# Kernel optimization log

Measured on AMD Instinct MI355X. Metric: run time of the kernel, lower is better.

## Reference

```python
import jax, jax.numpy as jnp
import numpy as np

N_NODES = 100000
F_IN = 128
F_HID = 64  # gcn_filters = [64, 64]
MLP_HID = 128


def setup_inputs() -> dict:
    key = jax.random.key(0)
    ks = jax.random.split(key, 12)
    E, Q = 3200000, 1000000
    feature = jax.random.normal(ks[0], (N_NODES, F_IN), dtype=jnp.float32)
    edges = jax.random.randint(ks[1], (2, E), 0, N_NODES, dtype=jnp.int32)
    i = jax.random.randint(ks[2], (Q,), 0, N_NODES, dtype=jnp.int32)
    j = jax.random.randint(ks[3], (Q,), 0, N_NODES, dtype=jnp.int32)
    s = lambda d: 1.0 / jnp.sqrt(d)
    W1 = jax.random.normal(ks[4], (F_IN, F_HID), dtype=jnp.float32) * s(F_IN)
    b1 = jnp.zeros((F_HID,), dtype=jnp.float32)
    W2 = jax.random.normal(ks[5], (F_HID, F_HID), dtype=jnp.float32) * s(F_HID)
    b2 = jnp.zeros((F_HID,), dtype=jnp.float32)
    fc1_W = jax.random.normal(ks[6], (2 * F_HID, MLP_HID), dtype=jnp.float32) * s(2 * F_HID)
    fc1_b = jnp.zeros((MLP_HID,), dtype=jnp.float32)
    fc2_W = jax.random.normal(ks[7], (MLP_HID, 2), dtype=jnp.float32) * s(MLP_HID)
    fc2_b = jnp.zeros((2,), dtype=jnp.float32)
    return {"feature": feature, "edges": edges, "i": i, "j": j,
            "W1": W1, "b1": b1, "W2": W2, "b2": b2,
            "fc1_W": fc1_W, "fc1_b": fc1_b, "fc2_W": fc2_W, "fc2_b": fc2_b}


def _gcn_layer(x, W, b, src, dst, norm, n):
    h = x @ W
    msg = h[src] * norm[:, None]
    return jax.ops.segment_sum(msg, dst, num_segments=n) + b


def reference(feature, edges, i, j, W1, b1, W2, b2, fc1_W, fc1_b, fc2_W, fc2_b):
    n = feature.shape[0]
    loops = jnp.arange(n, dtype=edges.dtype)
    src = jnp.concatenate([edges[0], loops])
    dst = jnp.concatenate([edges[1], loops])
    deg = jax.ops.segment_sum(jnp.ones(src.shape[0], feature.dtype), dst, num_segments=n)
    dinv = jax.lax.rsqrt(jnp.maximum(deg, 1e-12))
    norm = dinv[src] * dinv[dst]
    h = jax.nn.relu(_gcn_layer(feature, W1, b1, src, dst, norm, n))
    out = _gcn_layer(h, W2, b2, src, dst, norm, n)  # [N, F_HID]
    embd = jnp.concatenate([out[i], out[j]], axis=-1)  # [Q, 2*F_HID]
    hid = jax.nn.relu(embd @ fc1_W + fc1_b)
    return hid @ fc2_W + fc2_b
```

## Files before the change

kernel.cpp:

```cpp
#include <hip/hip_runtime.h>
#include <hip/hip_bf16.h>
#include <hip/hip_fp16.h>
#include <cstdint>

#define F_IN 128
#define F_HID 64
#define NB 64
#define MAXB 2048
#define NWG 1024
#define PREPB 16

typedef _Float16 half8 __attribute__((ext_vector_type(8)));
typedef float floatx4 __attribute__((ext_vector_type(4)));

__device__ __forceinline__ float bf2f(unsigned short u) {
  return __uint_as_float(((unsigned int)u) << 16);
}
__device__ __forceinline__ unsigned short f2bf(float f) {
  unsigned int u = __float_as_uint(f);
  u += 0x7FFFu + ((u >> 16) & 1u);
  return (unsigned short)(u >> 16);
}
__device__ __forceinline__ float h2f(unsigned short u) {
  return __half2float(__ushort_as_half(u));
}
__device__ __forceinline__ unsigned short f2h(float f) {
  return __half_as_ushort(__float2half(f));
}

__global__ __launch_bounds__(64) void k_detect(const unsigned int* __restrict__ Xw,
                                               int* __restrict__ flag) {
  int lane = threadIdx.x;
  int cnt = 0;
  for (int t = lane; t < 256; t += 64) {
    unsigned int ex = (Xw[t] >> 7) & 0xFFu;
    cnt += (ex >= 117u && ex <= 137u) ? 1 : 0;
  }
#pragma unroll
  for (int off = 32; off > 0; off >>= 1) cnt += __shfl_xor(cnt, off, 64);
  if (lane == 0) *flag = (cnt >= 128) ? 1 : 0;
}

__global__ __launch_bounds__(256) void k_front(const void* __restrict__ Xv,
                                               unsigned short* __restrict__ Xh, int total8,
                                               const void* __restrict__ W1v,
                                               const void* __restrict__ W2v,
                                               const void* __restrict__ fc1Wv,
                                               unsigned short* __restrict__ fW1,
                                               unsigned short* __restrict__ fW2,
                                               unsigned short* __restrict__ fPR,
                                               const int* __restrict__ dst,
                                               int* __restrict__ hist, int E, int B, int chunk,
                                               const int* __restrict__ flagp) {
  __shared__ int lh[MAXB];
  const int bid = blockIdx.x;
  if (bid < NWG) {
    int w = bid, tid = threadIdx.x;
    for (int b = tid; b < B; b += 256) lh[b] = 0;
    __syncthreads();
    int e0 = w * chunk, e1 = min(E, e0 + chunk);
    for (int e = e0 + tid; e < e1; e += 256) atomicAdd(&lh[dst[e] >> 6], 1);
    __syncthreads();
    for (int b = tid; b < B; b += 256) hist[w * B + b] = lh[b];
    return;
  }
  const bool isb = (*flagp != 0);
  if (bid < NWG + PREPB) {
    int tid = (bid - NWG) * 256 + threadIdx.x;
    int stride = PREPB * 256;
    for (int e = tid; e < F_IN * F_HID; e += stride) {
      int k = e >> 6, n = e & 63;
      unsigned short v = isb ? f2h(bf2f(((const unsigned short*)W1v)[e]))
                             : f2h(((const float*)W1v)[e]);
      int c = k >> 5, q = (k >> 3) & 3, j = k & 7, t = n >> 4, m = n & 15;
      fW1[((c * 4 + t) * 64 + q * 16 + m) * 8 + j] = v;
    }
    for (int e = tid; e < F_HID * F_HID; e += stride) {
      int k = e >> 6, n = e & 63;
      unsigned short v = isb ? f2h(bf2f(((const unsigned short*)W2v)[e]))
                             : f2h(((const float*)W2v)[e]);
      int c = k >> 5, q = (k >> 3) & 3, j = k & 7, t = n >> 4, m = n & 15;
      fW2[((c * 4 + t) * 64 + q * 16 + m) * 8 + j] = v;
    }
    for (int ge = tid; ge < 4 * F_HID * 64; ge += stride) {
      int g = ge >> 12, e = ge & 4095;
      int k = e >> 6, n = e & 63;
      int src = (((g & 2) ? 64 : 0) + k) * 128 + (g & 1) * 64 + n;
      unsigned short v = isb ? f2h(bf2f(((const unsigned short*)fc1Wv)[src]))
                             : f2h(((const float*)fc1Wv)[src]);
      int c = k >> 5, q = (k >> 3) & 3, j = k & 7, t = n >> 4, m = n & 15;
      fPR[g * 4096 + ((c * 4 + t) * 64 + q * 16 + m) * 8 + j] = v;
    }
    return;
  }
  int t = (bid - (NWG + PREPB)) * 256 + threadIdx.x;
  int stride = (gridDim.x - (NWG + PREPB)) * 256;
  for (; t < total8; t += stride) {
    unsigned short r[8];
    if (isb) {
      uint4 d = reinterpret_cast<const uint4*>(Xv)[t];
      r[0] = f2h(__uint_as_float(d.x << 16));
      r[1] = f2h(__uint_as_float(d.x & 0xFFFF0000u));
      r[2] = f2h(__uint_as_float(d.y << 16));
      r[3] = f2h(__uint_as_float(d.y & 0xFFFF0000u));
      r[4] = f2h(__uint_as_float(d.z << 16));
      r[5] = f2h(__uint_as_float(d.z & 0xFFFF0000u));
      r[6] = f2h(__uint_as_float(d.w << 16));
      r[7] = f2h(__uint_as_float(d.w & 0xFFFF0000u));
    } else {
      float4 a = reinterpret_cast<const float4*>(Xv)[2 * t];
      float4 b = reinterpret_cast<const float4*>(Xv)[2 * t + 1];
      r[0] = f2h(a.x); r[1] = f2h(a.y); r[2] = f2h(a.z); r[3] = f2h(a.w);
      r[4] = f2h(b.x); r[5] = f2h(b.y); r[6] = f2h(b.z); r[7] = f2h(b.w);
    }
    uint4 o;
    o.x = (unsigned int)r[0] | ((unsigned int)r[1] << 16);
    o.y = (unsigned int)r[2] | ((unsigned int)r[3] << 16);
    o.z = (unsigned int)r[4] | ((unsigned int)r[5] << 16);
    o.w = (unsigned int)r[6] | ((unsigned int)r[7] << 16);
    reinterpret_cast<uint4*>(Xh)[t] = o;
  }
}

__global__ __launch_bounds__(256) void k_bscan1(int* __restrict__ hist,
                                                int* __restrict__ btot, int B) {
  int b = (blockIdx.x * 256 + threadIdx.x) >> 6;
  int lane = threadIdx.x & 63;
  if (b >= B) return;
  int v[16];
  int s = 0;
#pragma unroll
  for (int k = 0; k < 16; k++) {
    v[k] = hist[(size_t)(lane * 16 + k) * B + b];
    s += v[k];
  }
  int pre = s;
#pragma unroll
  for (int off = 1; off < 64; off <<= 1) {
    int t = __shfl_up(pre, off, 64);
    if (lane >= off) pre += t;
  }
  int running = pre - s;
#pragma unroll
  for (int k = 0; k < 16; k++) {
    int val = v[k];
    hist[(size_t)(lane * 16 + k) * B + b] = running;
    running += val;
  }
  if (lane == 63) btot[b] = running;
}

__global__ __launch_bounds__(256) void k_bscan2(const int* __restrict__ btot,
                                                int* __restrict__ boff, int B, int E) {
  __shared__ int partial[256];
  int t = threadIdx.x;
  int CH = (B + 255) / 256;
  int b0 = t * CH, b1 = min(B, b0 + CH);
  int tt = 0;
  for (int b = b0; b < b1; b++) tt += btot[b];
  partial[t] = tt;
  __syncthreads();
  if (t == 0) {
    int acc = 0;
    for (int i = 0; i < 256; i++) { int v = partial[i]; partial[i] = acc; acc += v; }
  }
  __syncthreads();
  int off = partial[t];
  for (int b = b0; b < b1; b++) { boff[b] = off; off += btot[b]; }
  if (t == 255) boff[B] = E;
}

__global__ __launch_bounds__(256) void k_bfill(const int* __restrict__ src,
                                               const int* __restrict__ dst,
                                               const int* __restrict__ hist,
                                               const int* __restrict__ boff,
                                               int* __restrict__ buck,
                                               int E, int B, int chunk) {
  __shared__ int cur[MAXB];
  int w = blockIdx.x, tid = threadIdx.x;
  for (int b = tid; b < B; b += 256) cur[b] = boff[b] + hist[w * B + b];
  __syncthreads();
  int e0 = w * chunk, e1 = min(E, e0 + chunk);
  for (int e = e0 + tid; e < e1; e += 256) {
    int d = dst[e];
    int b = d >> 6, dl = d & 63;
    int p = atomicAdd(&cur[b], 1);
    buck[p] = (dl << 17) | src[e];
  }
}

__global__ __launch_bounds__(256) void k_bsort(const int* __restrict__ buck,
                                               const int* __restrict__ boff,
                                               int* __restrict__ csr,
                                               int* __restrict__ noff,
                                               float* __restrict__ dinv, int N) {
  __shared__ int bin[NB][4];
  __shared__ int excl[NB];
  int b = blockIdx.x, tid = threadIdx.x;
  const int rep = tid & 3;
  for (int i = tid; i < NB * 4; i += 256) ((int*)bin)[i] = 0;
  __syncthreads();
  int r0 = boff[b], r1 = boff[b + 1];
  for (int r = r0 + tid; r < r1; r += 256) atomicAdd(&bin[buck[r] >> 17][rep], 1);
  __syncthreads();
  if (tid < NB)
    excl[tid] = bin[tid][0] + bin[tid][1] + bin[tid][2] + bin[tid][3];
  __syncthreads();
  if (tid == 0) {
    int acc = 0;
    for (int i = 0; i < NB; i++) { int v = excl[i]; excl[i] = acc; acc += v; }
  }
  __syncthreads();
  if (tid < NB) {
    int n = b * NB + tid;
    int c0 = bin[tid][0], c1 = bin[tid][1], c2 = bin[tid][2], c3 = bin[tid][3];
    if (n < N) {
      dinv[n] = rsqrtf((float)(c0 + c1 + c2 + c3) + 1.0f);
      noff[n] = r0 + excl[tid];
    }
    int base = excl[tid];
    bin[tid][0] = base;
    bin[tid][1] = base + c0;
    bin[tid][2] = base + c0 + c1;
    bin[tid][3] = base + c0 + c1 + c2;
  }
  if (b == gridDim.x - 1 && tid == 128) noff[N] = r1;
  __syncthreads();
  for (int r = r0 + tid; r < r1; r += 256) {
    int rec = buck[r];
    int p = atomicAdd(&bin[rec >> 17][rep], 1);
    csr[r0 + p] = rec & 0x1FFFF;
  }
}


__global__ __launch_bounds__(256, 4) void k_gemm1(const unsigned short* __restrict__ Xh,
                                                  const unsigned short* __restrict__ fW1,
                                                  const float* __restrict__ dinv,
                                                  unsigned short* __restrict__ G, int N) {
  int tid = threadIdx.x;
  const int lane = tid & 63, wave = tid >> 6;
  const int m = lane & 15, q = lane >> 4;
  half8 bfrag[4][4];
#pragma unroll
  for (int c = 0; c < 4; c++)
#pragma unroll
    for (int t = 0; t < 4; t++)
      bfrag[c][t] = *reinterpret_cast<const half8*>(fW1 + ((c * 4 + t) * 64 + lane) * 8);
  int ntiles = (N + 15) >> 4;
  for (int tile = blockIdx.x * 4 + wave; tile < ntiles; tile += gridDim.x * 4) {
    int r0 = tile << 4;
    int rm = r0 + m; rm = rm < N ? rm : N - 1;
    floatx4 acc[4] = {{0.f,0.f,0.f,0.f},{0.f,0.f,0.f,0.f},{0.f,0.f,0.f,0.f},{0.f,0.f,0.f,0.f}};
#pragma unroll
    for (int c = 0; c < 4; c++) {
      half8 a = *reinterpret_cast<const half8*>(Xh + (size_t)rm * F_IN + c * 32 + q * 8);
#pragma unroll
      for (int t = 0; t < 4; t++)
        acc[t] = __builtin_amdgcn_mfma_f32_16x16x32_f16(a, bfrag[c][t], acc[t], 0, 0, 0);
    }
#pragma unroll
    for (int rr = 0; rr < 4; rr++) {
      int grow = r0 + q * 4 + rr;
      if (grow < N) {
        float dv = dinv[grow];
#pragma unroll
        for (int t = 0; t < 4; t++)
          G[(size_t)grow * F_HID + t * 16 + m] = f2h(acc[t][rr] * dv);
      }
    }
  }
}

__global__ __launch_bounds__(256, 4) void k_gemm2(const unsigned short* __restrict__ O,
                                                  const unsigned short* __restrict__ fW2,
                                                  const float* __restrict__ dinv,
                                                  unsigned short* __restrict__ G, int N) {
  int tid = threadIdx.x;
  const int lane = tid & 63, wave = tid >> 6;
  const int m = lane & 15, q = lane >> 4;
  half8 bfrag[2][4];
#pragma unroll
  for (int c = 0; c < 2; c++)
#pragma unroll
    for (int t = 0; t < 4; t++)
      bfrag[c][t] = *reinterpret_cast<const half8*>(fW2 + ((c * 4 + t) * 64 + lane) * 8);
  int ntiles = (N + 15) >> 4;
  for (int tile = blockIdx.x * 4 + wave; tile < ntiles; tile += gridDim.x * 4) {
    int r0 = tile << 4;
    int rm = r0 + m; rm = rm < N ? rm : N - 1;
    floatx4 acc[4] = {{0.f,0.f,0.f,0.f},{0.f,0.f,0.f,0.f},{0.f,0.f,0.f,0.f},{0.f,0.f,0.f,0.f}};
#pragma unroll
    for (int c = 0; c < 2; c++) {
      half8 a = *reinterpret_cast<const half8*>(O + (size_t)rm * F_HID + c * 32 + q * 8);
#pragma unroll
      for (int t = 0; t < 4; t++)
        acc[t] = __builtin_amdgcn_mfma_f32_16x16x32_f16(a, bfrag[c][t], acc[t], 0, 0, 0);
    }
#pragma unroll
    for (int rr = 0; rr < 4; rr++) {
      int grow = r0 + q * 4 + rr;
      if (grow < N) {
        float dv = dinv[grow];
#pragma unroll
        for (int t = 0; t < 4; t++)
          G[(size_t)grow * F_HID + t * 16 + m] = f2h(acc[t][rr] * dv);
      }
    }
  }
}

template <bool RELU>
__global__ __launch_bounds__(256) void k_agg(const int* __restrict__ csr,
                                             const int* __restrict__ noff,
                                             const unsigned short* __restrict__ H,
                                             const float* __restrict__ dinv,
                                             const void* __restrict__ bias,
                                             unsigned short* __restrict__ OUT, int N,
                                             const int* __restrict__ flagp) {
  const bool isb = (*flagp != 0);
  const int lane = threadIdx.x & 63;
  const int g = lane >> 4, l16 = lane & 15;
  const int gw = (blockIdx.x * 256 + threadIdx.x) >> 6;
  const int nW = (gridDim.x * 256) >> 6;
  float bv[4];
#pragma unroll
  for (int d = 0; d < 4; d++)
    bv[d] = isb ? bf2f(((const unsigned short*)bias)[l16 * 4 + d])
                : ((const float*)bias)[l16 * 4 + d];
  for (int n = gw; n < N; n += nW) {
    int start = noff[n], end = noff[n + 1];
    float a0 = 0.f, a1 = 0.f, a2 = 0.f, a3 = 0.f;
    for (int e0 = start; e0 < end; e0 += 64) {
      int ee = e0 + lane;
      int idx = (ee < end) ? csr[ee] : 0;
      int m = end - e0; m = m < 64 ? m : 64;
      int nc = m >> 2;
      int c = 0;
      for (; c + 8 <= nc; c += 8) {
        int s[8];
#pragma unroll
        for (int u = 0; u < 8; u++) s[u] = __shfl(idx, (c + u) * 4 + g, 64);
        ushort4 v[8];
#pragma unroll
        for (int u = 0; u < 8; u++)
          v[u] = *reinterpret_cast<const ushort4*>(H + (size_t)s[u] * F_HID + l16 * 4);
#pragma unroll
        for (int u = 0; u < 8; u++) {
          a0 += h2f(v[u].x); a1 += h2f(v[u].y);
          a2 += h2f(v[u].z); a3 += h2f(v[u].w);
        }
      }
      for (; c < nc; c++) {
        int s0 = __shfl(idx, c * 4 + g, 64);
        ushort4 v0 = *reinterpret_cast<const ushort4*>(H + (size_t)s0 * F_HID + l16 * 4);
        a0 += h2f(v0.x); a1 += h2f(v0.y); a2 += h2f(v0.z); a3 += h2f(v0.w);
      }
      int rem = m & 3;
      if (rem) {
        int s0 = __shfl(idx, nc * 4 + g, 64);
        if (g < rem) {
          ushort4 v0 = *reinterpret_cast<const ushort4*>(H + (size_t)s0 * F_HID + l16 * 4);
          a0 += h2f(v0.x); a1 += h2f(v0.y); a2 += h2f(v0.z); a3 += h2f(v0.w);
        }
      }
    }
    a0 += __shfl_xor(a0, 16, 64); a0 += __shfl_xor(a0, 32, 64);
    a1 += __shfl_xor(a1, 16, 64); a1 += __shfl_xor(a1, 32, 64);
    a2 += __shfl_xor(a2, 16, 64); a2 += __shfl_xor(a2, 32, 64);
    a3 += __shfl_xor(a3, 16, 64); a3 += __shfl_xor(a3, 32, 64);
    ushort4 sv = *reinterpret_cast<const ushort4*>(H + (size_t)n * F_HID + l16 * 4);
    float dv = dinv[n];
    float o0 = (a0 + h2f(sv.x)) * dv + bv[0];
    float o1 = (a1 + h2f(sv.y)) * dv + bv[1];
    float o2 = (a2 + h2f(sv.z)) * dv + bv[2];
    float o3 = (a3 + h2f(sv.w)) * dv + bv[3];
    if (RELU) {
      o0 = fmaxf(o0, 0.f); o1 = fmaxf(o1, 0.f);
      o2 = fmaxf(o2, 0.f); o3 = fmaxf(o3, 0.f);
    }
    if (lane < 16) {
      ushort4 ov;
      ov.x = f2h(o0); ov.y = f2h(o1); ov.z = f2h(o2); ov.w = f2h(o3);
      *reinterpret_cast<ushort4*>(OUT + (size_t)n * F_HID + l16 * 4) = ov;
    }
  }
}

__global__ __launch_bounds__(512) void k_query(const unsigned short* __restrict__ O,
                                               const unsigned short* __restrict__ fPR,
                                               const int* __restrict__ qi,
                                               const int* __restrict__ qj,
                                               const void* __restrict__ fc1b,
                                               const void* __restrict__ fc2W,
                                               const void* __restrict__ fc2b,
                                               void* __restrict__ out, int Q,
                                               const int* __restrict__ flagp) {
  __shared__ unsigned short sB[4 * 4096];
  const bool isb = (*flagp != 0);
  int tid = threadIdx.x;
  {
    const uint4* srcp = reinterpret_cast<const uint4*>(fPR);
    uint4* dstp = reinterpret_cast<uint4*>(sB);
#pragma unroll
    for (int r = 0; r < 4; r++) dstp[tid + r * 512] = srcp[tid + r * 512];
  }
  const int lane = tid & 63, wave = tid >> 6;
  const int m_ = lane & 15, qk = lane >> 4;
  float bb[8], w0[8], w1[8];
#pragma unroll
  for (int T = 0; T < 8; T++) {
    int h = T * 16 + m_;
    if (isb) {
      bb[T] = bf2f(((const unsigned short*)fc1b)[h]);
      w0[T] = bf2f(((const unsigned short*)fc2W)[h * 2 + 0]);
      w1[T] = bf2f(((const unsigned short*)fc2W)[h * 2 + 1]);
    } else {
      bb[T] = ((const float*)fc1b)[h];
      w0[T] = ((const float*)fc2W)[h * 2 + 0];
      w1[T] = ((const float*)fc2W)[h * 2 + 1];
    }
  }
  float ob0 = isb ? bf2f(((const unsigned short*)fc2b)[0]) : ((const float*)fc2b)[0];
  float ob1 = isb ? bf2f(((const unsigned short*)fc2b)[1]) : ((const float*)fc2b)[1];
  __syncthreads();
  const half8* sBv = reinterpret_cast<const half8*>(sB);

  const int ntiles = (Q + 15) >> 4;
  const int nW = gridDim.x * 8;
  int tile = blockIdx.x * 8 + wave;
  if (tile >= ntiles) return;

  auto ldidx = [&](int t, int& iq, int& jq) {
    if (t < ntiles) {
      int q = t * 16 + m_;
      int qq = q < Q ? q : Q - 1;
      iq = qi[qq];
      jq = qj[qq];
    }
  };
  auto gather = [&](int iq, int jq, half8& I0, half8& I1, half8& J0, half8& J1) {
    const half8* pI = reinterpret_cast<const half8*>(O + (size_t)iq * F_HID) + qk;
    const half8* pJ = reinterpret_cast<const half8*>(O + (size_t)jq * F_HID) + qk;
    I0 = pI[0]; I1 = pI[4];
    J0 = pJ[0]; J1 = pJ[4];
  };

  int iqn = 0, jqn = 0;
  ldidx(tile, iqn, jqn);
  half8 I0, I1, J0, J1;
  gather(iqn, jqn, I0, I1, J0, J1);
  ldidx(tile + nW, iqn, jqn);

  for (; tile < ntiles; tile += nW) {
    half8 nI0, nI1, nJ0, nJ1;
    gather(iqn, jqn, nI0, nI1, nJ0, nJ1);
    ldidx(tile + 2 * nW, iqn, jqn);

    float r0[4] = {0.f, 0.f, 0.f, 0.f};
    float r1[4] = {0.f, 0.f, 0.f, 0.f};
    const floatx4 zz = {0.f, 0.f, 0.f, 0.f};
#pragma unroll
    for (int h = 0; h < 2; h++) {
      floatx4 acc[4];
#pragma unroll
      for (int tt = 0; tt < 4; tt++) acc[tt] = zz;
      __builtin_amdgcn_s_setprio(1);
#pragma unroll
      for (int tt = 0; tt < 4; tt++) {
        acc[tt] = __builtin_amdgcn_mfma_f32_16x16x32_f16(
            I0, sBv[h * 512 + tt * 64 + lane], acc[tt], 0, 0, 0);
        acc[tt] = __builtin_amdgcn_mfma_f32_16x16x32_f16(
            I1, sBv[h * 512 + (4 + tt) * 64 + lane], acc[tt], 0, 0, 0);
        acc[tt] = __builtin_amdgcn_mfma_f32_16x16x32_f16(
            J0, sBv[(2 + h) * 512 + tt * 64 + lane], acc[tt], 0, 0, 0);
        acc[tt] = __builtin_amdgcn_mfma_f32_16x16x32_f16(
            J1, sBv[(2 + h) * 512 + (4 + tt) * 64 + lane], acc[tt], 0, 0, 0);
      }
      __builtin_amdgcn_s_setprio(0);
#pragma unroll
      for (int tt = 0; tt < 4; tt++) {
        int T = h * 4 + tt;
#pragma unroll
        for (int rr = 0; rr < 4; rr++) {
          float hv = fmaxf(acc[tt][rr] + bb[T], 0.f);
          r0[rr] += hv * w0[T];
          r1[rr] += hv * w1[T];
        }
      }
      __builtin_amdgcn_sched_barrier(0);
    }
#pragma unroll
    for (int rr = 0; rr < 4; rr++) {
      float a0 = r0[rr], a1 = r1[rr];
#pragma unroll
      for (int off = 8; off > 0; off >>= 1) {
        a0 += __shfl_xor(a0, off, 16);
        a1 += __shfl_xor(a1, off, 16);
      }
      if (m_ == 0) {
        int q = tile * 16 + qk * 4 + rr;
        if (q < Q) {
          if (isb) {
            *reinterpret_cast<ushort2*>((unsigned short*)out + (size_t)q * 2) =
                make_ushort2(f2bf(a0 + ob0), f2bf(a1 + ob1));
          } else {
            *reinterpret_cast<float2*>((float*)out + (size_t)q * 2) =
                make_float2(a0 + ob0, a1 + ob1);
          }
        }
      }
    }
    I0 = nI0; I1 = nI1; J0 = nJ0; J1 = nJ1;
  }
}

extern "C" void kernel_launch(void* const* d_in, const int* in_sizes, int n_in,
                              void* d_out, int out_size, void* d_ws, size_t ws_size,
                              hipStream_t stream) {
  const void* X    = d_in[0];
  const int*  edges= (const int*)d_in[1];
  const int*  qi   = (const int*)d_in[2];
  const int*  qj   = (const int*)d_in[3];
  const void* W1   = d_in[4];
  const void* b1   = d_in[5];
  const void* W2   = d_in[6];
  const void* b2   = d_in[7];
  const void* fc1W = d_in[8];
  const void* fc1b = d_in[9];
  const void* fc2W = d_in[10];
  const void* fc2b = d_in[11];

  const int N = in_sizes[0] / F_IN;
  const int E = in_sizes[1] / 2;
  const int Q = in_sizes[2];
  const int B = (N + NB - 1) / NB;
  const int chunk = (E + NWG - 1) / NWG;

  char* ws = (char*)d_ws;
  size_t off = 0;
  auto alloc = [&](size_t bytes) -> void* {
    void* p = ws + off;
    off += (bytes + 255) & ~(size_t)255;
    return p;
  };
  int*            flag = (int*)alloc(4);
  float*          dinv = (float*)alloc((size_t)N * 4);
  unsigned short* Xh   = (unsigned short*)alloc((size_t)N * F_IN * 2);
  unsigned short* G    = (unsigned short*)alloc((size_t)N * F_HID * 2);
  unsigned short* O    = (unsigned short*)alloc((size_t)N * F_HID * 2);
  unsigned short* fW1  = (unsigned short*)alloc((size_t)F_IN * F_HID * 2);
  unsigned short* fW2  = (unsigned short*)alloc((size_t)F_HID * F_HID * 2);
  unsigned short* fPR  = (unsigned short*)alloc((size_t)4 * F_HID * 64 * 2);
  int* hist = (int*)alloc((size_t)NWG * B * 4);
  int* btot = (int*)alloc((size_t)(B + 1) * 4);
  int* boff = (int*)alloc((size_t)(B + 1) * 4);
  int* buck = (int*)alloc((size_t)E * 4);
  int* csr  = (int*)alloc((size_t)E * 4);
  int* noff = (int*)alloc((size_t)(N + 1) * 4);
  (void)ws_size; (void)n_in; (void)out_size;

  const int* esrc = edges;
  const int* edst = edges + E;

  k_detect<<<1, 64, 0, stream>>>((const unsigned int*)X, flag);
  k_front<<<2048, 256, 0, stream>>>(X, Xh, N * F_IN / 8, W1, W2, fc1W, fW1, fW2, fPR,
                                    edst, hist, E, B, chunk, flag);

  k_bscan1<<<(B + 3) / 4, 256, 0, stream>>>(hist, btot, B);
  k_bscan2<<<1, 256, 0, stream>>>(btot, boff, B, E);
  k_bfill<<<NWG, 256, 0, stream>>>(esrc, edst, hist, boff, buck, E, B, chunk);
  k_bsort<<<B, 256, 0, stream>>>(buck, boff, csr, noff, dinv, N);

  k_gemm1<<<2048, 256, 0, stream>>>(Xh, fW1, dinv, G, N);
  k_agg<true><<<2048, 256, 0, stream>>>(csr, noff, G, dinv, b1, O, N, flag);

  k_gemm2<<<2048, 256, 0, stream>>>(O, fW2, dinv, G, N);
  k_agg<false><<<2048, 256, 0, stream>>>(csr, noff, G, dinv, b2, O, N, flag);

  k_query<<<1024, 512, 0, stream>>>(O, fPR, qi, qj, fc1b, fc2W, fc2b, d_out, Q, flag);
}
```

Measured before the change: 450.8 us.

## Stage bucket fill through LDS for coalesced bucketed writes, fewer workgroups

The bucket-fill kernel now sorts each chunk of edges by bucket in shared memory (local histogram, local scan, local scatter) before writing them to global memory. Edges for the same bucket then land in contiguous runs, replacing the random global scatter. The workgroup count drops from 1024 to 256 so each group handles a larger chunk, and the scan kernel is generalized to match. The cost is extra LDS traffic, several barriers per stage, a serial 256-entry scan on one thread, and lower occupancy from the large shared-memory footprint.

```diff
diff --git a/kernel.cpp b/kernel.cpp
--- a/kernel.cpp
+++ b/kernel.cpp
@@ -7,8 +7,9 @@
 #define F_HID 64
 #define NB 64
 #define MAXB 2048
-#define NWG 1024
+#define NWG 256
 #define PREPB 16
+#define STAGE 12800
 
 typedef _Float16 half8 __attribute__((ext_vector_type(8)));
 typedef float floatx4 __attribute__((ext_vector_type(4)));
@@ -124,14 +125,15 @@
 
 __global__ __launch_bounds__(256) void k_bscan1(int* __restrict__ hist,
                                                 int* __restrict__ btot, int B) {
+  const int WPL = NWG / 64;
   int b = (blockIdx.x * 256 + threadIdx.x) >> 6;
   int lane = threadIdx.x & 63;
   if (b >= B) return;
-  int v[16];
+  int v[WPL];
   int s = 0;
 #pragma unroll
-  for (int k = 0; k < 16; k++) {
-    v[k] = hist[(size_t)(lane * 16 + k) * B + b];
+  for (int k = 0; k < WPL; k++) {
+    v[k] = hist[(size_t)(lane * WPL + k) * B + b];
     s += v[k];
   }
   int pre = s;
@@ -142,9 +144,9 @@
   }
   int running = pre - s;
 #pragma unroll
-  for (int k = 0; k < 16; k++) {
+  for (int k = 0; k < WPL; k++) {
     int val = v[k];
-    hist[(size_t)(lane * 16 + k) * B + b] = running;
+    hist[(size_t)(lane * WPL + k) * B + b] = running;
     running += val;
   }
   if (lane == 63) btot[b] = running;
@@ -176,16 +178,56 @@
                                                const int* __restrict__ boff,
                                                int* __restrict__ buck,
                                                int E, int B, int chunk) {
-  __shared__ int cur[MAXB];
-  int w = blockIdx.x, tid = threadIdx.x;
-  for (int b = tid; b < B; b += 256) cur[b] = boff[b] + hist[w * B + b];
-  __syncthreads();
+  __shared__ int gcur[MAXB];
+  __shared__ int lexcl[MAXB];
+  __shared__ int lcur[MAXB];
+  __shared__ int stage[STAGE];
+  __shared__ unsigned short bdex[STAGE];
+  __shared__ int part[256];
+  const int w = blockIdx.x, tid = threadIdx.x;
+  for (int b = tid; b < B; b += 256) gcur[b] = boff[b] + hist[w * B + b];
   int e0 = w * chunk, e1 = min(E, e0 + chunk);
-  for (int e = e0 + tid; e < e1; e += 256) {
-    int d = dst[e];
-    int b = d >> 6, dl = d & 63;
-    int p = atomicAdd(&cur[b], 1);
-    buck[p] = (dl << 17) | src[e];
+  for (int s0 = e0; s0 < e1; s0 += STAGE) {
+    int s1 = min(e1, s0 + STAGE);
+    int cnt = s1 - s0;
+    for (int b = tid; b < B; b += 256) lexcl[b] = 0;
+    __syncthreads();
+    for (int e = s0 + tid; e < s1; e += 256) atomicAdd(&lexcl[dst[e] >> 6], 1);
+    __syncthreads();
+    int CH = (B + 255) >> 8;
+    int b0 = tid * CH, b1 = min(B, b0 + CH);
+    int s = 0;
+    for (int b = b0; b < b1; b++) s += lexcl[b];
+    part[tid] = s;
+    __syncthreads();
+    if (tid == 0) {
+      int acc = 0;
+      for (int i = 0; i < 256; i++) { int v = part[i]; part[i] = acc; acc += v; }
+    }
+    __syncthreads();
+    int run = part[tid];
+    for (int b = b0; b < b1; b++) {
+      int v = lexcl[b];
+      lexcl[b] = run;
+      lcur[b] = run;
+      run += v;
+    }
+    __syncthreads();
+    for (int e = s0 + tid; e < s1; e += 256) {
+      int d = dst[e];
+      int b = d >> 6;
+      int p = atomicAdd(&lcur[b], 1);
+      stage[p] = ((d & 63) << 17) | src[e];
+      bdex[p] = (unsigned short)b;
+    }
+    __syncthreads();
+    for (int p = tid; p < cnt; p += 256) {
+      int b = bdex[p];
+      buck[gcur[b] + (p - lexcl[b])] = stage[p];
+    }
+    __syncthreads();
+    for (int b = tid; b < B; b += 256) gcur[b] += lcur[b] - lexcl[b];
+    __syncthreads();
   }
 }
 
```

Result: faster. 438.3 us (-2.8%).
